# Kernel optimization log

Hardware: AMD Instinct MI355X
Metric: run time of the kernel (lower is better)

Reference implementation:

```python
import jax, jax.numpy as jnp
import numpy as np

B, T, H, V = 32, 256, 1024, 256


def setup_inputs() -> dict:
    key = jax.random.key(0)
    ks = jax.random.split(key, 12)
    xavier = float(np.sqrt(6.0 / (H + V)))
    inp = {
        "x": jax.random.randint(ks[0], (B, T), 0, V, dtype=jnp.int64),
        "targets": jax.random.randint(ks[1], (B, T), 0, V, dtype=jnp.int64),
        "h0": jnp.zeros((B, H), jnp.float32),
        "c0": jnp.zeros((B, H), jnp.float32),
        "h1": jnp.zeros((B, H), jnp.float32),
        "c1": jnp.zeros((B, H), jnp.float32),
        # learned params
        "emb": jax.random.normal(ks[2], (V, H), jnp.float32) * 0.05,
        "W_ih0": jax.random.normal(ks[3], (H, 4 * H), jnp.float32) / np.sqrt(H),
        "W_hh0": jax.random.normal(ks[4], (H, 4 * H), jnp.float32) / np.sqrt(H),
        "b0": jnp.zeros((4 * H,), jnp.float32),
        "W_ih1": jax.random.normal(ks[5], (H, 4 * H), jnp.float32) / np.sqrt(H),
        "W_hh1": jax.random.normal(ks[6], (H, 4 * H), jnp.float32) / np.sqrt(H),
        "b1": jnp.zeros((4 * H,), jnp.float32),
        "W_out": jax.random.uniform(ks[7], (H, V), jnp.float32, -xavier, xavier),
        "b_out": jnp.zeros((V,), jnp.float32),
    }
    return inp


def _lstm_cell(h, c, inp, W_ih, W_hh, b):
    # gates: [B, 4H] -> i, f, g, o
    z = inp @ W_ih + h @ W_hh + b
    i, f, g, o = jnp.split(z, 4, axis=-1)
    c_new = jax.nn.sigmoid(f) * c + jax.nn.sigmoid(i) * jnp.tanh(g)
    h_new = jax.nn.sigmoid(o) * jnp.tanh(c_new)
    return h_new, c_new


def reference(x, targets, h0, c0, h1, c1, emb, W_ih0, W_hh0, b0,
              W_ih1, W_hh1, b1, W_out, b_out):
    # Teacher-forcing branch: embed targets, feed embedding at every step.
    embeddings = emb[targets]            # [B, T, H]
    e_seq = jnp.swapaxes(embeddings, 0, 1)  # [T, B, H] for scan over time

    def step(carry, e_t):
        (h0, c0), (h1, c1) = carry
        h0, c0 = _lstm_cell(h0, c0, e_t, W_ih0, W_hh0, b0)
        h1, c1 = _lstm_cell(h1, c1, h0, W_ih1, W_hh1, b1)
        logit = h1 @ W_out + b_out       # [B, V]
        return ((h0, c0), (h1, c1)), logit

    carry0 = ((h0, c0), (h1, c1))
    carry_f, logits_tbv = jax.lax.scan(step, carry0, e_seq)
    logits = jnp.swapaxes(logits_tbv, 0, 1)  # [B, T, V]
    (h0f, c0f), (h1f, c1f) = carry_f
    return logits, h0f, c0f, h1f, c1f
```

## Files before the change

### kernel.cpp

```cpp
#include <hip/hip_runtime.h>
#include <cstdint>


typedef float    f32x4 __attribute__((ext_vector_type(4)));
typedef short    s16x8 __attribute__((ext_vector_type(8)));
typedef unsigned u32x4 __attribute__((ext_vector_type(4)));

#define DEV __device__ __forceinline__

DEV unsigned short f2bf(float x){
  unsigned u = __builtin_bit_cast(unsigned, x);
  unsigned r = (u + 0x7fffu + ((u >> 16) & 1u)) >> 16;
  return (unsigned short)r;
}
DEV float bf2f(unsigned short b){ return __builtin_bit_cast(float, ((unsigned)b) << 16); }

DEV s16x8 ld16(const void* p){ return *(const s16x8*)p; }

DEV f32x4 MF(s16x8 a, s16x8 b, f32x4 c){
  return __builtin_amdgcn_mfma_f32_16x16x32_bf16(a, b, c, 0, 0, 0);
}

#define LDC(dst, ptr)  asm volatile("global_load_dwordx4 %0, %1, off sc0 sc1" : "=v"(dst) : "v"(ptr))
#define LDP(dst, ptr)  asm volatile("global_load_dwordx4 %0, %1, off"         : "=v"(dst) : "v"(ptr))
#define WAITVM(n) do { asm volatile("s_waitcnt vmcnt(" #n ")" ::: "memory"); \
                       __builtin_amdgcn_sched_barrier(0); } while (0)
#define CFENCE()  asm volatile("" ::: "memory")
#define TRIPLE(Cmn, Ahm, Alm, Bhn, Bln) do { \
    Cmn = MF(Ahm, Bhn, Cmn); Cmn = MF(Ahm, Bln, Cmn); Cmn = MF(Alm, Bhn, Cmn); } while (0)

DEV void st16c(void* p, u32x4 v){
  asm volatile("global_store_dwordx4 %0, %1, off sc0 sc1" :: "v"(p), "v"(v) : "memory");
}
DEV void st16cf(void* p, f32x4 v){ st16c(p, __builtin_bit_cast(u32x4, v)); }
DEV void set_flag(int* p, int v){
  __hip_atomic_store(p, v, __ATOMIC_RELAXED, __HIP_MEMORY_SCOPE_AGENT);
}
template<int SLP>
DEV void pollT(const int* f, int lane, int target){
  const int* p0 = f + lane * 8;
  const int* p1 = f + (64 + lane) * 8;
  for (;;) {
    int a = __hip_atomic_load(p0, __ATOMIC_RELAXED, __HIP_MEMORY_SCOPE_AGENT);
    int b = __hip_atomic_load(p1, __ATOMIC_RELAXED, __HIP_MEMORY_SCOPE_AGENT);
    if (__all((a >= target) && (b >= target))) break;
    __builtin_amdgcn_s_sleep(SLP);
  }
  CFENCE();
}
DEV void pollC(const int* f1p, int t1, const int* f2p, int t2, int lane){
  const int* a = f1p + lane * 8;
  const int* b = f2p + lane * 8;
  for (;;) {
    int x = __hip_atomic_load(a, __ATOMIC_RELAXED, __HIP_MEMORY_SCOPE_AGENT);
    int y = __hip_atomic_load(b, __ATOMIC_RELAXED, __HIP_MEMORY_SCOPE_AGENT);
    if (__all((x >= t1) && (y >= t2))) break;
    __builtin_amdgcn_s_sleep(1);
  }
  CFENCE();
}
DEV void pollB(const int* f0p, int t0, const int* f2p, int t2,
               const int* f1p, int t1, int lane){
  const int* a0 = f0p + lane * 8;
  const int* a1 = f0p + (64 + lane) * 8;
  const int* b  = f2p + lane * 8;
  const int* c  = f1p + lane * 8;
  for (;;) {
    int x0 = __hip_atomic_load(a0, __ATOMIC_RELAXED, __HIP_MEMORY_SCOPE_AGENT);
    int x1 = __hip_atomic_load(a1, __ATOMIC_RELAXED, __HIP_MEMORY_SCOPE_AGENT);
    int y  = __hip_atomic_load(b,  __ATOMIC_RELAXED, __HIP_MEMORY_SCOPE_AGENT);
    int z  = __hip_atomic_load(c,  __ATOMIC_RELAXED, __HIP_MEMORY_SCOPE_AGENT);
    if (__all((x0 >= t0) && (x1 >= t0) && (y >= t2) && (z >= t1))) break;
    __builtin_amdgcn_s_sleep(2);
  }
  CFENCE();
}
DEV char* h0slot(char* wa0, char* s0, char* hi, int s){
  return (s == 0) ? s0 : ((s <= 128) ? wa0 + ((size_t)(s - 1) << 17)
                                     : hi  + ((size_t)(s - 129) << 17));
}

DEV void gemm16u(const char* smemA, const char* ALb, int jb0, const char* Bb,
                 int ksb, int lane, f32x4 (&C)[4][2]) {
  s16x8 P[3][4], AL[3][4];
  #pragma unroll
  for (int d = 0; d < 2; ++d) {
    #pragma unroll
    for (int q = 0; q < 4; ++q) LDP(P[d][q], Bb + ((q * 32 + ksb + d) << 10) + lane * 16);
    #pragma unroll
    for (int m = 0; m < 4; ++m)
      LDP(AL[d][m], ALb + ((((jb0 + m) * 2 + 1) * 32 + ksb + d) << 10) + lane * 16);
  }
  #pragma unroll
  for (int i = 0; i < 8; ++i) {
    const int ks = ksb + i;
    if (i < 6) {
      #pragma unroll
      for (int q = 0; q < 4; ++q) LDP(P[(i + 2) % 3][q], Bb + ((q * 32 + ks + 2) << 10) + lane * 16);
      #pragma unroll
      for (int m = 0; m < 4; ++m)
        LDP(AL[(i + 2) % 3][m], ALb + ((((jb0 + m) * 2 + 1) * 32 + ks + 2) << 10) + lane * 16);
    }
    s16x8 Ah[4];
    #pragma unroll
    for (int m = 0; m < 4; ++m) Ah[m] = ld16(smemA + ((m * 32 + ks) << 10) + lane * 16);
    if (i < 6) { WAITVM(16); } else if (i == 6) { WAITVM(8); } else { WAITVM(0); }
    #pragma unroll
    for (int m = 0; m < 4; ++m) {
      TRIPLE(C[m][0], Ah[m], AL[i % 3][m], P[i % 3][0], P[i % 3][2]);
      TRIPLE(C[m][1], Ah[m], AL[i % 3][m], P[i % 3][1], P[i % 3][3]);
    }
  }
}

__global__ void prep_wfrag(const float* __restrict__ W0, const float* __restrict__ W1,
                           const float* __restrict__ W2, const float* __restrict__ W3,
                           char* D0, char* D1, char* D2, char* D3) {
  int gid = blockIdx.x * 256 + threadIdx.x;
  int lane = gid & 63, ks = (gid >> 6) & 31, jb = (gid >> 11) & 255, mat = gid >> 19;
  const float* S = (mat == 0) ? W0 : (mat == 1) ? W1 : (mat == 2) ? W2 : W3;
  char* D = (mat == 0) ? D0 : (mat == 1) ? D1 : (mat == 2) ? D2 : D3;
  int jp = jb * 16 + (lane & 15), u = jp >> 2, g = jp & 3;
  int kb = ks * 32 + (lane >> 4) * 8;
  s16x8 vh, vl;
  #pragma unroll
  for (int i = 0; i < 8; ++i) {
    float x = S[(kb + i) * 4096 + g * 1024 + u];
    unsigned short h = f2bf(x);
    vh[i] = (short)h;
    vl[i] = (short)f2bf(x - bf2f(h));
  }
  *(s16x8*)(D + (((jb * 2 + 0) * 32 + ks) << 10) + lane * 16) = vh;
  *(s16x8*)(D + (((jb * 2 + 1) * 32 + ks) << 10) + lane * 16) = vl;
}

__global__ void prep_bfrag(const float* __restrict__ emb, const float* __restrict__ Wout,
                           char* Demb, char* Dwout) {
  int gid = blockIdx.x * 256 + threadIdx.x;
  int lane = gid & 63, ks = (gid >> 6) & 31, vb = (gid >> 11) & 15, which = gid >> 15;
  int v = vb * 16 + (lane & 15), kb = ks * 32 + (lane >> 4) * 8;
  s16x8 vh, vl;
  #pragma unroll
  for (int i = 0; i < 8; ++i) {
    float x = which ? Wout[(kb + i) * 256 + v] : emb[v * 1024 + kb + i];
    unsigned short h = f2bf(x);
    vh[i] = (short)h;
    vl[i] = (short)f2bf(x - bf2f(h));
  }
  char* D = which ? Dwout : Demb;
  *(s16x8*)(D + (((vb * 2 + 0) * 32 + ks) << 10) + lane * 16) = vh;
  *(s16x8*)(D + (((vb * 2 + 1) * 32 + ks) << 10) + lane * 16) = vl;
}

__global__ void prep_hinit(const float* __restrict__ h0, const float* __restrict__ h1,
                           char* h0s0, char* h1f) {
  int gid = blockIdx.x * 256 + threadIdx.x;
  int lane = gid & 63, ks = (gid >> 6) & 31, nt = (gid >> 11) & 1, which = gid >> 12;
  const float* S = which ? h1 : h0;
  char* D = which ? h1f : h0s0;
  int b = nt * 16 + (lane & 15), kb = ks * 32 + (lane >> 4) * 8;
  s16x8 vh, vl;
  #pragma unroll
  for (int i = 0; i < 8; ++i) {
    float x = S[b * 1024 + kb + i];
    unsigned short h = f2bf(x);
    vh[i] = (short)h;
    vl[i] = (short)f2bf(x - bf2f(h));
  }
  *(s16x8*)(D + (((0 * 2 + nt) * 32 + ks) << 10) + lane * 16) = vh;
  *(s16x8*)(D + (((1 * 2 + nt) * 32 + ks) << 10) + lane * 16) = vl;
}

__global__ void prep_misc(const float* __restrict__ b1, float* b1i,
                          int* f0a, int* f1a, int* f2a) {
  int i = blockIdx.x * 256 + threadIdx.x;
  if (i < 4096) b1i[i] = b1[(i & 3) * 1024 + (i >> 2)];
  if (i < 1024) {
    f0a[i] = -1;
    f1a[i] = (i >= 512) ? 0x7fffffff : -1;
    f2a[i] = (i >= 512) ? 0x7fffffff : -1;
  }
}

__global__ __launch_bounds__(256, 1) void lstm_persist(
    const int* __restrict__ tgt,
    const float* __restrict__ c0_in, const float* __restrict__ c1_in,
    const float* __restrict__ b0, const float* __restrict__ b_out,
    char* __restrict__ WA0, const char* __restrict__ WA1, const char* __restrict__ WA2,
    const char* __restrict__ WAi0, const char* __restrict__ WoutB, const char* __restrict__ embB,
    float* __restrict__ E0, const float* __restrict__ b1i,
    char* __restrict__ h0s0, char* __restrict__ h0hi, char* __restrict__ h1frag,
    char* __restrict__ z1ring,
    int* __restrict__ f0, int* __restrict__ f1, int* __restrict__ f2,
    float* __restrict__ out)
{
  extern __shared__ char smem[];
  constexpr int PARTA = 131072;
  constexpr int RP0   = 147456;
  constexpr int PARTB = 131072;
  constexpr int RP1   = 155648;
  const int tid = threadIdx.x, lane = tid & 63, wv = tid >> 6;
  const int wg = blockIdx.x;
  const int l15 = lane & 15, l4 = lane >> 4;

  __builtin_amdgcn_fence(__ATOMIC_ACQUIRE, "agent");

  if (wg < 128) {
    const int wgl = wg;
    const int mi_e = wv >> 1, nt_e = wv & 1;
    {
      u32x4 tmp[8];
      for (int blk = 0; blk < 4; ++blk) {
        #pragma unroll
        for (int q = 0; q < 8; ++q) {
          int idx = tid + (blk * 8 + q) * 256;
          int l16 = idx & 63, ks = (idx >> 6) & 31, mi = (idx >> 11) & 1, part = idx >> 12;
          LDC(tmp[q], WA0 + ((((wgl * 2 + mi) * 2 + part) * 32 + ks) << 10) + l16 * 16);
        }
        WAITVM(0);
        #pragma unroll
        for (int q = 0; q < 8; ++q) {
          int idx = tid + (blk * 8 + q) * 256;
          int l16 = idx & 63, ks = (idx >> 6) & 31, mi = (idx >> 11) & 1, part = idx >> 12;
          *(u32x4*)(smem + (((part * 2 + mi) * 32 + ks) << 10) + l16 * 16) = tmp[q];
        }
      }
    }
    {
      f32x4 C[2][4];
      #pragma unroll
      for (int a = 0; a < 2; ++a)
        #pragma unroll
        for (int b = 0; b < 4; ++b) C[a][b] = 0.0f;
      for (int ks = 0; ks < 32; ++ks) {
        s16x8 Ah0, Ah1, Al0, Al1;
        LDC(Ah0, WAi0 + ((((wgl * 2 + 0) * 2 + 0) * 32 + ks) << 10) + lane * 16);
        LDC(Ah1, WAi0 + ((((wgl * 2 + 1) * 2 + 0) * 32 + ks) << 10) + lane * 16);
        LDC(Al0, WAi0 + ((((wgl * 2 + 0) * 2 + 1) * 32 + ks) << 10) + lane * 16);
        LDC(Al1, WAi0 + ((((wgl * 2 + 1) * 2 + 1) * 32 + ks) << 10) + lane * 16);
        WAITVM(0);
        #pragma unroll
        for (int v4 = 0; v4 < 4; ++v4) {
          int vb = wv * 4 + v4;
          s16x8 Bh = ld16(embB + (((vb * 2 + 0) * 32 + ks) << 10) + lane * 16);
          s16x8 Bl = ld16(embB + (((vb * 2 + 1) * 32 + ks) << 10) + lane * 16);
          TRIPLE(C[0][v4], Ah0, Al0, Bh, Bl);
          TRIPLE(C[1][v4], Ah1, Al1, Bh, Bl);
        }
      }
      #pragma unroll
      for (int mi = 0; mi < 2; ++mi) {
        int jb4 = wgl * 32 + mi * 16 + l4 * 4;
        int u = jb4 >> 2;
        f32x4 bb;
        #pragma unroll
        for (int r = 0; r < 4; ++r) bb[r] = b0[r * 1024 + u];
        #pragma unroll
        for (int v4 = 0; v4 < 4; ++v4) {
          int v = (wv * 4 + v4) * 16 + l15;
          *(f32x4*)(E0 + v * 4096 + jb4) = C[mi][v4] + bb;
        }
      }
    }
    float cst = c0_in[(nt_e * 16 + l15) * 1024 + wgl * 8 + mi_e * 4 + l4];
    __syncthreads();
    if (tid == 0) set_flag(f0 + wgl * 8, 0);

    for (int t = 0; t < 256; ++t) {
      const int s = t + 1;
      f32x4 C[2][2];
      #pragma unroll
      for (int a = 0; a < 2; ++a)
        #pragma unroll
        for (int b = 0; b < 2; ++b) C[a][b] = 0.0f;
      int tv = tgt[(nt_e * 16 + l15) * 256 + t];
      f32x4 e0v = *(const f32x4*)(E0 + (size_t)tv * 4096 + wgl * 32 + mi_e * 16 + (l4 << 2));
      pollT<1>(f0, lane, t);
      const char* Bb = h0slot(WA0, h0s0, h0hi, t);
      const int ksb = wv * 8;
      s16x8 P[3][4];
      #pragma unroll
      for (int d = 0; d < 2; ++d)
        #pragma unroll
        for (int q = 0; q < 4; ++q) LDP(P[d][q], Bb + ((q * 32 + ksb + d) << 10) + lane * 16);
      #pragma unroll
      for (int i = 0; i < 8; ++i) {
        const int ks = ksb + i;
        if (i < 6) {
          #pragma unroll
          for (int q = 0; q < 4; ++q) LDP(P[(i + 2) % 3][q], Bb + ((q * 32 + ks + 2) << 10) + lane * 16);
        }
        s16x8 Ah0 = ld16(smem + ((0 * 32 + ks) << 10) + lane * 16);
        s16x8 Ah1 = ld16(smem + ((1 * 32 + ks) << 10) + lane * 16);
        s16x8 Al0 = ld16(smem + ((2 * 32 + ks) << 10) + lane * 16);
        s16x8 Al1 = ld16(smem + ((3 * 32 + ks) << 10) + lane * 16);
        if (i < 6) { WAITVM(8); } else if (i == 6) { WAITVM(4); } else { WAITVM(0); }
        TRIPLE(C[0][0], Ah0, Al0, P[i % 3][0], P[i % 3][2]);
        TRIPLE(C[0][1], Ah0, Al0, P[i % 3][1], P[i % 3][3]);
        TRIPLE(C[1][0], Ah1, Al1, P[i % 3][0], P[i % 3][2]);
        TRIPLE(C[1][1], Ah1, Al1, P[i % 3][1], P[i % 3][3]);
      }
      #pragma unroll
      for (int mi = 0; mi < 2; ++mi)
        #pragma unroll
        for (int nt = 0; nt < 2; ++nt)
          *(f32x4*)(smem + PARTA + ((wv * 4 + mi * 2 + nt) << 10) + lane * 16) = C[mi][nt];
      __syncthreads();
      {
        f32x4 z = *(const f32x4*)(smem + PARTA + ((0 * 4 + wv) << 10) + lane * 16);
        #pragma unroll
        for (int w = 1; w < 4; ++w)
          z += *(const f32x4*)(smem + PARTA + ((w * 4 + wv) << 10) + lane * 16);
        z += e0v;
        float ig = 1.f / (1.f + __expf(-z[0]));
        float fg = 1.f / (1.f + __expf(-z[1]));
        float og = 1.f / (1.f + __expf(-z[3]));
        float cn = fg * cst + ig * tanhf(z[2]);
        float hn = og * tanhf(cn);
        cst = cn;
        unsigned short hb = f2bf(hn);
        unsigned short lb = f2bf(hn - bf2f(hb));
        *(short*)(smem + RP0 + ((0 + nt_e) * 16 + l15) * 16 + (mi_e * 4 + l4) * 2) = (short)hb;
        *(short*)(smem + RP0 + ((2 + nt_e) * 16 + l15) * 16 + (mi_e * 4 + l4) * 2) = (short)lb;
        if (t == 255) {
          int u = wgl * 8 + mi_e * 4 + l4, b = nt_e * 16 + l15;
          out[2097152 + b * 1024 + u] = hn;
          out[2097152 + 32768 + b * 1024 + u] = cn;
        }
      }
      __syncthreads();
      if (wv == 0) {
        char* hd = h0slot(WA0, h0s0, h0hi, s);
        u32x4 v = *(const u32x4*)(smem + RP0 + lane * 16);
        char* dst = hd + (((lane >> 4) * 32 + (wgl >> 2)) << 10) + ((wgl & 3) * 16 + l15) * 16;
        st16c(dst, v);
        asm volatile("s_waitcnt vmcnt(0)" ::: "memory");
        if (lane == 0) set_flag(f0 + wgl * 8, s);
      }
    }
  } else if (wg < 192) {
    const int wgb = wg - 128;
    const int jb0 = wgb * 4;
    for (int idx = tid; idx < 8192; idx += 256) {
      int l16 = idx & 63, ks = (idx >> 6) & 31, m = idx >> 11;
      u32x4 v = *(const u32x4*)(WA1 + ((((jb0 + m) * 2 + 0) * 32 + ks) << 10) + l16 * 16);
      *(u32x4*)(smem + ((m * 32 + ks) << 10) + l16 * 16) = v;
    }
    __syncthreads();
    if (tid == 0) set_flag(f2 + wgb * 8, 0);

    for (int t = 0; t < 256; ++t) {
      const int rt = (t >= 4) ? (t - 3) : 0;
      pollB(f0, t + 1, f2, t, f1, rt, lane);
      f32x4 Cb[4][2];
      #pragma unroll
      for (int a = 0; a < 4; ++a)
        #pragma unroll
        for (int b = 0; b < 2; ++b) Cb[a][b] = 0.0f;
      gemm16u(smem, WA1, jb0, h0slot(WA0, h0s0, h0hi, t + 1), wv * 8, lane, Cb);
      if (wv) {
        #pragma unroll
        for (int m = 0; m < 4; ++m)
          #pragma unroll
          for (int n = 0; n < 2; ++n)
            *(f32x4*)(smem + PARTB + (((wv - 1) * 8 + m * 2 + n) << 10) + lane * 16) = Cb[m][n];
      }
      __syncthreads();
      if (wv == 0) {
        char* zs = z1ring + ((size_t)(t & 3) * 64 + wgb) * 8192;
        #pragma unroll
        for (int m = 0; m < 4; ++m)
          #pragma unroll
          for (int n = 0; n < 2; ++n) {
            f32x4 z = Cb[m][n];
            #pragma unroll
            for (int w = 1; w < 4; ++w)
              z += *(const f32x4*)(smem + PARTB + (((w - 1) * 8 + m * 2 + n) << 10) + lane * 16);
            st16cf(zs + ((m * 2 + n) * 64 + lane) * 16, z);
          }
        asm volatile("s_waitcnt vmcnt(0)" ::: "memory");
        if (lane == 0) set_flag(f2 + wgb * 8, t + 1);
      }
    }
  } else {
    const int wgc = wg - 192;
    const int jb0 = wgc * 4;
    for (int idx = tid; idx < 8192; idx += 256) {
      int l16 = idx & 63, ks = (idx >> 6) & 31, m = idx >> 11;
      u32x4 v = *(const u32x4*)(WA2 + ((((jb0 + m) * 2 + 0) * 32 + ks) << 10) + l16 * 16);
      *(u32x4*)(smem + ((m * 32 + ks) << 10) + l16 * 16) = v;
    }
    f32x4 b1z4[4];
    float cst[4][2];
    if (wv == 0) {
      #pragma unroll
      for (int m = 0; m < 4; ++m) {
        b1z4[m] = *(const f32x4*)(b1i + wgc * 64 + m * 16 + (l4 << 2));
        #pragma unroll
        for (int n = 0; n < 2; ++n)
          cst[m][n] = c1_in[(n * 16 + l15) * 1024 + wgc * 16 + m * 4 + l4];
      }
    }
    __syncthreads();
    if (tid == 0) set_flag(f1 + wgc * 8, 0);

    for (int t = 0; t < 256; ++t) {
      const int s = t + 1;
      pollC(f1, t, f2, s, lane);
      f32x4 zA[4][2];
      if (wv == 0) {
        const char* zs = z1ring + ((size_t)(t & 3) * 64 + wgc) * 8192;
        #pragma unroll
        for (int m = 0; m < 4; ++m)
          #pragma unroll
          for (int n = 0; n < 2; ++n)
            LDC(zA[m][n], zs + ((m * 2 + n) * 64 + lane) * 16);
      }
      f32x4 Cc[4][2];
      #pragma unroll
      for (int a = 0; a < 4; ++a)
        #pragma unroll
        for (int b = 0; b < 2; ++b) Cc[a][b] = 0.0f;
      gemm16u(smem, WA2, jb0, h1frag + (size_t)t * 131072, wv * 8, lane, Cc);
      if (wv) {
        #pragma unroll
        for (int m = 0; m < 4; ++m)
          #pragma unroll
          for (int n = 0; n < 2; ++n)
            *(f32x4*)(smem + PARTB + (((wv - 1) * 8 + m * 2 + n) << 10) + lane * 16) = Cc[m][n];
      }
      __syncthreads();
      if (wv == 0) {
        #pragma unroll
        for (int m = 0; m < 4; ++m)
          #pragma unroll
          for (int n = 0; n < 2; ++n) {
            f32x4 z = Cc[m][n];
            #pragma unroll
            for (int w = 1; w < 4; ++w)
              z += *(const f32x4*)(smem + PARTB + (((w - 1) * 8 + m * 2 + n) << 10) + lane * 16);
            z += zA[m][n] + b1z4[m];
            float ig = 1.f / (1.f + __expf(-z[0]));
            float fg = 1.f / (1.f + __expf(-z[1]));
            float og = 1.f / (1.f + __expf(-z[3]));
            float cn = fg * cst[m][n] + ig * tanhf(z[2]);
            float hn = og * tanhf(cn);
            cst[m][n] = cn;
            unsigned short hb = f2bf(hn);
            unsigned short lb = f2bf(hn - bf2f(hb));
            int i8 = (m * 4 + l4) & 7, subl = (m * 4 + l4) >> 3;
            *(short*)(smem + RP1 + (((0 * 2 + n) * 2 + subl) * 16 + l15) * 16 + i8 * 2) = (short)hb;
            *(short*)(smem + RP1 + (((1 * 2 + n) * 2 + subl) * 16 + l15) * 16 + i8 * 2) = (short)lb;
            if (t == 255) {
              int u = wgc * 16 + m * 4 + l4, b = n * 16 + l15;
              out[2097152 + 65536 + b * 1024 + u] = hn;
              out[2097152 + 98304 + b * 1024 + u] = cn;
            }
          }
        char* hd = h1frag + (size_t)s * 131072;
        asm volatile("s_waitcnt lgkmcnt(0)" ::: "memory");
        __builtin_amdgcn_sched_barrier(0);
        #pragma unroll
        for (int h = 0; h < 2; ++h) {
          int idx16 = lane * 2 + h;
          u32x4 v = *(const u32x4*)(smem + RP1 + idx16 * 16);
          int l15r = idx16 & 15, subl = (idx16 >> 4) & 1, ntq = (idx16 >> 5) & 1, part = idx16 >> 6;
          char* dst = hd + (((part * 2 + ntq) * 32 + (wgc >> 1)) << 10)
                         + (((wgc & 1) * 2 + subl) * 16 + l15r) * 16;
          st16c(dst, v);
        }
        asm volatile("s_waitcnt vmcnt(0)" ::: "memory");
        if (lane == 0) set_flag(f1 + wgc * 8, s);
      }
    }
  }

  {
    const int tp = wg;
    pollT<32>(f1, lane, tp + 1);
    const char* A = h1frag + (size_t)(tp + 1) * 131072;
    f32x4 C[2][4];
    #pragma unroll
    for (int a = 0; a < 2; ++a)
      #pragma unroll
      for (int b = 0; b < 4; ++b) C[a][b] = 0.0f;
    s16x8 QA[4], QB[4];
    #pragma unroll
    for (int q = 0; q < 4; ++q) LDP(QA[q], A + ((q * 32 + 0) << 10) + lane * 16);
    for (int kk = 0; kk < 16; ++kk) {
      const int ks = kk * 2;
      #pragma unroll
      for (int q = 0; q < 4; ++q) LDP(QB[q], A + ((q * 32 + ks + 1) << 10) + lane * 16);
      asm volatile("s_waitcnt vmcnt(4)" ::: "memory");
      __builtin_amdgcn_sched_barrier(0);
      #pragma unroll
      for (int v4 = 0; v4 < 4; ++v4) {
        int vb = wv * 4 + v4;
        s16x8 Bh = ld16(WoutB + (((vb * 2 + 0) * 32 + ks) << 10) + lane * 16);
        s16x8 Bl = ld16(WoutB + (((vb * 2 + 1) * 32 + ks) << 10) + lane * 16);
        C[0][v4] = MF(QA[0], Bh, C[0][v4]); C[0][v4] = MF(QA[0], Bl, C[0][v4]); C[0][v4] = MF(QA[2], Bh, C[0][v4]);
        C[1][v4] = MF(QA[1], Bh, C[1][v4]); C[1][v4] = MF(QA[1], Bl, C[1][v4]); C[1][v4] = MF(QA[3], Bh, C[1][v4]);
      }
      if (kk < 15) {
        #pragma unroll
        for (int q = 0; q < 4; ++q) LDP(QA[q], A + ((q * 32 + ks + 2) << 10) + lane * 16);
        asm volatile("s_waitcnt vmcnt(4)" ::: "memory");
      } else {
        asm volatile("s_waitcnt vmcnt(0)" ::: "memory");
      }
      __builtin_amdgcn_sched_barrier(0);
      #pragma unroll
      for (int v4 = 0; v4 < 4; ++v4) {
        int vb = wv * 4 + v4;
        s16x8 Bh = ld16(WoutB + (((vb * 2 + 0) * 32 + ks + 1) << 10) + lane * 16);
        s16x8 Bl = ld16(WoutB + (((vb * 2 + 1) * 32 + ks + 1) << 10) + lane * 16);
        C[0][v4] = MF(QB[0], Bh, C[0][v4]); C[0][v4] = MF(QB[0], Bl, C[0][v4]); C[0][v4] = MF(QB[2], Bh, C[0][v4]);
        C[1][v4] = MF(QB[1], Bh, C[1][v4]); C[1][v4] = MF(QB[1], Bl, C[1][v4]); C[1][v4] = MF(QB[3], Bh, C[1][v4]);
      }
    }
    #pragma unroll
    for (int nt = 0; nt < 2; ++nt)
      #pragma unroll
      for (int v4 = 0; v4 < 4; ++v4) {
        int v = (wv * 4 + v4) * 16 + l15;
        float bo = b_out[v];
        #pragma unroll
        for (int r = 0; r < 4; ++r) {
          int b = nt * 16 + l4 * 4 + r;
          out[((size_t)b * 256 + tp) * 256 + v] = C[nt][v4][r] + bo;
        }
      }
  }
}

extern "C" void kernel_launch(void* const* d_in, const int* in_sizes, int n_in,
                              void* d_out, int out_size, void* d_ws, size_t ws_size,
                              hipStream_t stream) {
  const int*   targets = (const int*)d_in[1];
  const float* h0_in   = (const float*)d_in[2];
  const float* c0_in   = (const float*)d_in[3];
  const float* h1_in   = (const float*)d_in[4];
  const float* c1_in   = (const float*)d_in[5];
  const float* emb     = (const float*)d_in[6];
  const float* W_ih0   = (const float*)d_in[7];
  const float* W_hh0   = (const float*)d_in[8];
  const float* b0      = (const float*)d_in[9];
  const float* W_ih1   = (const float*)d_in[10];
  const float* W_hh1   = (const float*)d_in[11];
  const float* b1      = (const float*)d_in[12];
  const float* W_out   = (const float*)d_in[13];
  const float* b_out   = (const float*)d_in[14];
  float* out = (float*)d_out;

  char* ws = (char*)d_ws;
  char*  WA0    = ws;
  char*  WA1    = ws + 16777216;
  char*  WA2    = ws + 33554432;
  char*  WoutB  = ws + 50331648;
  char*  embB   = ws + 51380224;
  float* E0     = (float*)(ws + 52428800);
  float* b1i    = (float*)(ws + 56623104);
  int*   f0     = (int*)(ws + 56639488);
  int*   f1     = (int*)(ws + 56643584);
  char*  h0s0   = ws + 56647680;
  char*  h0hi   = ws + 56778752;
  char*  h1frag = ws + 73555968;
  char*  z1ring = ws + 107241472;
  int*   f2     = (int*)(ws + 109338624);
  char*  WAi0   = h1frag + 16777216;

  prep_misc <<<18,   256, 0, stream>>>(b1, b1i, f0, f1, f2);
  prep_wfrag<<<8192, 256, 0, stream>>>(W_hh0, W_ih1, W_hh1, W_ih0, WA0, WA1, WA2, WAi0);
  prep_bfrag<<<256,  256, 0, stream>>>(emb, W_out, embB, WoutB);
  prep_hinit<<<32,   256, 0, stream>>>(h0_in, h1_in, h0s0, h1frag);

  hipFuncSetAttribute(reinterpret_cast<const void*>(lstm_persist),
                      hipFuncAttributeMaxDynamicSharedMemorySize, 157696);
  lstm_persist<<<256, 256, 157696, stream>>>(
      targets, c0_in, c1_in, b0, b_out,
      WA0, WA1, WA2, WAi0, WoutB, embB,
      E0, b1i, h0s0, h0hi, h1frag, z1ring, f0, f1, f2, out);
}
```

Baseline: 2.106 ms.

## Rebalance persistent LSTM roles: fewer layer-0 blocks, more layer-1 recurrent blocks

Reassigns the 256 persistent workgroups so that layer 0 uses 64 blocks, each owning 64 gate columns, while the layer-1 recurrent stage uses 128 blocks with 32 columns each. Before this, layer 0 had 128 blocks and layer-1 recurrence had 64. Layer-0 blocks now run the shared gemm16u routine over a 4-tile slice of W_hh0. Layer-1 blocks use the split-K pipelined inner loop with hi/lo weights held in LDS. Workspace slots, flag layouts and poll helpers are rearranged to match, including h1 history slots placed in reused weight buffers. The aim is to shorten the layer-1 recurrent critical path, at the cost of more work per layer-0 block, which could lengthen layer 0's recurrence instead.

```diff
diff --git a/kernel.cpp b/kernel.cpp
--- a/kernel.cpp
+++ b/kernel.cpp
@@ -35,6 +35,16 @@
 DEV void st16cf(void* p, f32x4 v){ st16c(p, __builtin_bit_cast(u32x4, v)); }
 DEV void set_flag(int* p, int v){
   __hip_atomic_store(p, v, __ATOMIC_RELAXED, __HIP_MEMORY_SCOPE_AGENT);
+}
+template<int SLP>
+DEV void poll64(const int* f, int lane, int target){
+  const int* p = f + lane * 8;
+  for (;;) {
+    int a = __hip_atomic_load(p, __ATOMIC_RELAXED, __HIP_MEMORY_SCOPE_AGENT);
+    if (__all(a >= target)) break;
+    __builtin_amdgcn_s_sleep(SLP);
+  }
+  CFENCE();
 }
 template<int SLP>
 DEV void pollT(const int* f, int lane, int target){
@@ -48,36 +58,34 @@
   }
   CFENCE();
 }
-DEV void pollC(const int* f1p, int t1, const int* f2p, int t2, int lane){
-  const int* a = f1p + lane * 8;
-  const int* b = f2p + lane * 8;
-  for (;;) {
-    int x = __hip_atomic_load(a, __ATOMIC_RELAXED, __HIP_MEMORY_SCOPE_AGENT);
-    int y = __hip_atomic_load(b, __ATOMIC_RELAXED, __HIP_MEMORY_SCOPE_AGENT);
-    if (__all((x >= t1) && (y >= t2))) break;
-    __builtin_amdgcn_s_sleep(1);
-  }
-  CFENCE();
-}
 DEV void pollB(const int* f0p, int t0, const int* f2p, int t2,
                const int* f1p, int t1, int lane){
-  const int* a0 = f0p + lane * 8;
-  const int* a1 = f0p + (64 + lane) * 8;
+  const int* a = f0p + lane * 8;
+  const int* b = f2p + lane * 8;
+  const int* c0 = f1p + lane * 8;
+  const int* c1 = f1p + (64 + lane) * 8;
+  for (;;) {
+    int x = __hip_atomic_load(a,  __ATOMIC_RELAXED, __HIP_MEMORY_SCOPE_AGENT);
+    int y = __hip_atomic_load(b,  __ATOMIC_RELAXED, __HIP_MEMORY_SCOPE_AGENT);
+    int z0 = __hip_atomic_load(c0, __ATOMIC_RELAXED, __HIP_MEMORY_SCOPE_AGENT);
+    int z1 = __hip_atomic_load(c1, __ATOMIC_RELAXED, __HIP_MEMORY_SCOPE_AGENT);
+    if (__all((x >= t0) && (y >= t2) && (z0 >= t1) && (z1 >= t1))) break;
+    __builtin_amdgcn_s_sleep(2);
+  }
+  CFENCE();
+}
+DEV void pollC(const int* f1p, int t1, const int* f2p, int t2, int lane){
+  const int* a0 = f1p + lane * 8;
+  const int* a1 = f1p + (64 + lane) * 8;
   const int* b  = f2p + lane * 8;
-  const int* c  = f1p + lane * 8;
   for (;;) {
     int x0 = __hip_atomic_load(a0, __ATOMIC_RELAXED, __HIP_MEMORY_SCOPE_AGENT);
     int x1 = __hip_atomic_load(a1, __ATOMIC_RELAXED, __HIP_MEMORY_SCOPE_AGENT);
     int y  = __hip_atomic_load(b,  __ATOMIC_RELAXED, __HIP_MEMORY_SCOPE_AGENT);
-    int z  = __hip_atomic_load(c,  __ATOMIC_RELAXED, __HIP_MEMORY_SCOPE_AGENT);
-    if (__all((x0 >= t0) && (x1 >= t0) && (y >= t2) && (z >= t1))) break;
-    __builtin_amdgcn_s_sleep(2);
+    if (__all((x0 >= t1) && (x1 >= t1) && (y >= t2))) break;
+    __builtin_amdgcn_s_sleep(1);
   }
   CFENCE();
-}
-DEV char* h0slot(char* wa0, char* s0, char* hi, int s){
-  return (s == 0) ? s0 : ((s <= 128) ? wa0 + ((size_t)(s - 1) << 17)
-                                     : hi  + ((size_t)(s - 129) << 17));
 }
 
 DEV void gemm16u(const char* smemA, const char* ALb, int jb0, const char* Bb,
@@ -153,11 +161,11 @@
 }
 
 __global__ void prep_hinit(const float* __restrict__ h0, const float* __restrict__ h1,
-                           char* h0s0, char* h1f) {
+                           char* h0s0, char* h1s0) {
   int gid = blockIdx.x * 256 + threadIdx.x;
   int lane = gid & 63, ks = (gid >> 6) & 31, nt = (gid >> 11) & 1, which = gid >> 12;
   const float* S = which ? h1 : h0;
-  char* D = which ? h1f : h0s0;
+  char* D = which ? h1s0 : h0s0;
   int b = nt * 16 + (lane & 15), kb = ks * 32 + (lane >> 4) * 8;
   s16x8 vh, vl;
   #pragma unroll
@@ -175,82 +183,70 @@
                           int* f0a, int* f1a, int* f2a) {
   int i = blockIdx.x * 256 + threadIdx.x;
   if (i < 4096) b1i[i] = b1[(i & 3) * 1024 + (i >> 2)];
-  if (i < 1024) {
-    f0a[i] = -1;
-    f1a[i] = (i >= 512) ? 0x7fffffff : -1;
-    f2a[i] = (i >= 512) ? 0x7fffffff : -1;
-  }
+  if (i < 1024) { f0a[i] = -1; f1a[i] = -1; f2a[i] = -1; }
 }
 
 __global__ __launch_bounds__(256, 1) void lstm_persist(
     const int* __restrict__ tgt,
     const float* __restrict__ c0_in, const float* __restrict__ c1_in,
     const float* __restrict__ b0, const float* __restrict__ b_out,
-    char* __restrict__ WA0, const char* __restrict__ WA1, const char* __restrict__ WA2,
-    const char* __restrict__ WAi0, const char* __restrict__ WoutB, const char* __restrict__ embB,
+    const char* __restrict__ WA0, const char* __restrict__ WA1, char* __restrict__ WA2,
+    char* __restrict__ WAi0, const char* __restrict__ WoutB, const char* __restrict__ embB,
     float* __restrict__ E0, const float* __restrict__ b1i,
-    char* __restrict__ h0s0, char* __restrict__ h0hi, char* __restrict__ h1frag,
-    char* __restrict__ z1ring,
+    char* __restrict__ h0all, char* __restrict__ h1s0, char* __restrict__ z1ring,
     int* __restrict__ f0, int* __restrict__ f1, int* __restrict__ f2,
     float* __restrict__ out)
 {
   extern __shared__ char smem[];
-  constexpr int PARTA = 131072;
-  constexpr int RP0   = 147456;
-  constexpr int PARTB = 131072;
-  constexpr int RP1   = 155648;
+  constexpr int PARTAB = 131072;
+  constexpr int RPA    = 155648;
+  constexpr int PARTC  = 131072;
+  constexpr int RPC    = 143360;
   const int tid = threadIdx.x, lane = tid & 63, wv = tid >> 6;
   const int wg = blockIdx.x;
   const int l15 = lane & 15, l4 = lane >> 4;
 
+  auto h1slot = [&](int s) -> char* {
+    return (s == 0) ? h1s0 : ((s <= 128) ? WA2 + ((size_t)(s - 1) << 17)
+                                         : WAi0 + ((size_t)(s - 129) << 17));
+  };
+  auto h0slot = [&](int s) -> char* { return h0all + ((size_t)s << 17); };
+
   __builtin_amdgcn_fence(__ATOMIC_ACQUIRE, "agent");
 
-  if (wg < 128) {
+  if (wg < 64) {
     const int wgl = wg;
-    const int mi_e = wv >> 1, nt_e = wv & 1;
+    for (int idx = tid; idx < 8192; idx += 256) {
+      int l16 = idx & 63, ks = (idx >> 6) & 31, m = idx >> 11;
+      u32x4 v = *(const u32x4*)(WA0 + ((((wgl * 4 + m) * 2 + 0) * 32 + ks) << 10) + l16 * 16);
+      *(u32x4*)(smem + ((m * 32 + ks) << 10) + l16 * 16) = v;
+    }
     {
-      u32x4 tmp[8];
-      for (int blk = 0; blk < 4; ++blk) {
-        #pragma unroll
-        for (int q = 0; q < 8; ++q) {
-          int idx = tid + (blk * 8 + q) * 256;
-          int l16 = idx & 63, ks = (idx >> 6) & 31, mi = (idx >> 11) & 1, part = idx >> 12;
-          LDC(tmp[q], WA0 + ((((wgl * 2 + mi) * 2 + part) * 32 + ks) << 10) + l16 * 16);
-        }
-        WAITVM(0);
-        #pragma unroll
-        for (int q = 0; q < 8; ++q) {
-          int idx = tid + (blk * 8 + q) * 256;
-          int l16 = idx & 63, ks = (idx >> 6) & 31, mi = (idx >> 11) & 1, part = idx >> 12;
-          *(u32x4*)(smem + (((part * 2 + mi) * 32 + ks) << 10) + l16 * 16) = tmp[q];
-        }
-      }
-    }
-    {
-      f32x4 C[2][4];
-      #pragma unroll
-      for (int a = 0; a < 2; ++a)
+      f32x4 C[4][4];
+      #pragma unroll
+      for (int a = 0; a < 4; ++a)
         #pragma unroll
         for (int b = 0; b < 4; ++b) C[a][b] = 0.0f;
       for (int ks = 0; ks < 32; ++ks) {
-        s16x8 Ah0, Ah1, Al0, Al1;
-        LDC(Ah0, WAi0 + ((((wgl * 2 + 0) * 2 + 0) * 32 + ks) << 10) + lane * 16);
-        LDC(Ah1, WAi0 + ((((wgl * 2 + 1) * 2 + 0) * 32 + ks) << 10) + lane * 16);
-        LDC(Al0, WAi0 + ((((wgl * 2 + 0) * 2 + 1) * 32 + ks) << 10) + lane * 16);
-        LDC(Al1, WAi0 + ((((wgl * 2 + 1) * 2 + 1) * 32 + ks) << 10) + lane * 16);
+        s16x8 Ah[4], Al[4];
+        #pragma unroll
+        for (int m = 0; m < 4; ++m) {
+          LDC(Ah[m], WAi0 + ((((wgl * 4 + m) * 2 + 0) * 32 + ks) << 10) + lane * 16);
+          LDC(Al[m], WAi0 + ((((wgl * 4 + m) * 2 + 1) * 32 + ks) << 10) + lane * 16);
+        }
         WAITVM(0);
         #pragma unroll
         for (int v4 = 0; v4 < 4; ++v4) {
           int vb = wv * 4 + v4;
           s16x8 Bh = ld16(embB + (((vb * 2 + 0) * 32 + ks) << 10) + lane * 16);
           s16x8 Bl = ld16(embB + (((vb * 2 + 1) * 32 + ks) << 10) + lane * 16);
-          TRIPLE(C[0][v4], Ah0, Al0, Bh, Bl);
-          TRIPLE(C[1][v4], Ah1, Al1, Bh, Bl);
-        }
-      }
-      #pragma unroll
-      for (int mi = 0; mi < 2; ++mi) {
-        int jb4 = wgl * 32 + mi * 16 + l4 * 4;
+          #pragma unroll
+          for (int m = 0; m < 4; ++m) TRIPLE(C[m][v4], Ah[m], Al[m], Bh, Bl);
+        }
+      }
+      #pragma unroll
+      for (int m = 0; m < 4; ++m) {
+        int jb4 = wgl * 64 + m * 16 + l4 * 4;
         int u = jb4 >> 2;
         f32x4 bb;
         #pragma unroll
@@ -258,188 +254,58 @@
         #pragma unroll
         for (int v4 = 0; v4 < 4; ++v4) {
           int v = (wv * 4 + v4) * 16 + l15;
-          *(f32x4*)(E0 + v * 4096 + jb4) = C[mi][v4] + bb;
-        }
-      }
-    }
-    float cst = c0_in[(nt_e * 16 + l15) * 1024 + wgl * 8 + mi_e * 4 + l4];
+          *(f32x4*)(E0 + v * 4096 + jb4) = C[m][v4] + bb;
+        }
+      }
+    }
+    float cst[4][2];
+    if (wv == 0) {
+      #pragma unroll
+      for (int m = 0; m < 4; ++m)
+        #pragma unroll
+        for (int n = 0; n < 2; ++n)
+          cst[m][n] = c0_in[(n * 16 + l15) * 1024 + wgl * 16 + m * 4 + l4];
+    }
     __syncthreads();
     if (tid == 0) set_flag(f0 + wgl * 8, 0);
 
     for (int t = 0; t < 256; ++t) {
       const int s = t + 1;
-      f32x4 C[2][2];
-      #pragma unroll
-      for (int a = 0; a < 2; ++a)
+      f32x4 e0v[4][2];
+      if (wv == 0) {
+        #pragma unroll
+        for (int n = 0; n < 2; ++n) {
+          int tv = tgt[(n * 16 + l15) * 256 + t];
+          #pragma unroll
+          for (int m = 0; m < 4; ++m)
+            e0v[m][n] = *(const f32x4*)(E0 + (size_t)tv * 4096 + wgl * 64 + m * 16 + (l4 << 2));
+        }
+      }
+      poll64<1>(f0, lane, t);
+      f32x4 C[4][2];
+      #pragma unroll
+      for (int a = 0; a < 4; ++a)
         #pragma unroll
         for (int b = 0; b < 2; ++b) C[a][b] = 0.0f;
-      int tv = tgt[(nt_e * 16 + l15) * 256 + t];
-      f32x4 e0v = *(const f32x4*)(E0 + (size_t)tv * 4096 + wgl * 32 + mi_e * 16 + (l4 << 2));
-      pollT<1>(f0, lane, t);
-      const char* Bb = h0slot(WA0, h0s0, h0hi, t);
-      const int ksb = wv * 8;
-      s16x8 P[3][4];
-      #pragma unroll
-      for (int d = 0; d < 2; ++d)
-        #pragma unroll
-        for (int q = 0; q < 4; ++q) LDP(P[d][q], Bb + ((q * 32 + ksb + d) << 10) + lane * 16);
-      #pragma unroll
-      for (int i = 0; i < 8; ++i) {
-        const int ks = ksb + i;
-        if (i < 6) {
-          #pragma unroll
-          for (int q = 0; q < 4; ++q) LDP(P[(i + 2) % 3][q], Bb + ((q * 32 + ks + 2) << 10) + lane * 16);
-        }
-        s16x8 Ah0 = ld16(smem + ((0 * 32 + ks) << 10) + lane * 16);
-        s16x8 Ah1 = ld16(smem + ((1 * 32 + ks) << 10) + lane * 16);
-        s16x8 Al0 = ld16(smem + ((2 * 32 + ks) << 10) + lane * 16);
-        s16x8 Al1 = ld16(smem + ((3 * 32 + ks) << 10) + lane * 16);
-        if (i < 6) { WAITVM(8); } else if (i == 6) { WAITVM(4); } else { WAITVM(0); }
-        TRIPLE(C[0][0], Ah0, Al0, P[i % 3][0], P[i % 3][2]);
-        TRIPLE(C[0][1], Ah0, Al0, P[i % 3][1], P[i % 3][3]);
-        TRIPLE(C[1][0], Ah1, Al1, P[i % 3][0], P[i % 3][2]);
-        TRIPLE(C[1][1], Ah1, Al1, P[i % 3][1], P[i % 3][3]);
-      }
-      #pragma unroll
-      for (int mi = 0; mi < 2; ++mi)
-        #pragma unroll
-        for (int nt = 0; nt < 2; ++nt)
-          *(f32x4*)(smem + PARTA + ((wv * 4 + mi * 2 + nt) << 10) + lane * 16) = C[mi][nt];
-      __syncthreads();
-      {
-        f32x4 z = *(const f32x4*)(smem + PARTA + ((0 * 4 + wv) << 10) + lane * 16);
-        #pragma unroll
-        for (int w = 1; w < 4; ++w)
-          z += *(const f32x4*)(smem + PARTA + ((w * 4 + wv) << 10) + lane * 16);
-        z += e0v;
-        float ig = 1.f / (1.f + __expf(-z[0]));
-        float fg = 1.f / (1.f + __expf(-z[1]));
-        float og = 1.f / (1.f + __expf(-z[3]));
-        float cn = fg * cst + ig * tanhf(z[2]);
-        float hn = og * tanhf(cn);
-        cst = cn;
-        unsigned short hb = f2bf(hn);
-        unsigned short lb = f2bf(hn - bf2f(hb));
-        *(short*)(smem + RP0 + ((0 + nt_e) * 16 + l15) * 16 + (mi_e * 4 + l4) * 2) = (short)hb;
-        *(short*)(smem + RP0 + ((2 + nt_e) * 16 + l15) * 16 + (mi_e * 4 + l4) * 2) = (short)lb;
-        if (t == 255) {
-          int u = wgl * 8 + mi_e * 4 + l4, b = nt_e * 16 + l15;
-          out[2097152 + b * 1024 + u] = hn;
-          out[2097152 + 32768 + b * 1024 + u] = cn;
-        }
+      gemm16u(smem, WA0, wgl * 4, h0slot(t), wv * 8, lane, C);
+      if (wv) {
+        #pragma unroll
+        for (int m = 0; m < 4; ++m)
+          #pragma unroll
+          for (int n = 0; n < 2; ++n)
+            *(f32x4*)(smem + PARTAB + (((wv - 1) * 8 + m * 2 + n) << 10) + lane * 16) = C[m][n];
       }
       __syncthreads();
       if (wv == 0) {
-        char* hd = h0slot(WA0, h0s0, h0hi, s);
-        u32x4 v = *(const u32x4*)(smem + RP0 + lane * 16);
-        char* dst = hd + (((lane >> 4) * 32 + (wgl >> 2)) << 10) + ((wgl & 3) * 16 + l15) * 16;
-        st16c(dst, v);
-        asm volatile("s_waitcnt vmcnt(0)" ::: "memory");
-        if (lane == 0) set_flag(f0 + wgl * 8, s);
-      }
-    }
-  } else if (wg < 192) {
-    const int wgb = wg - 128;
-    const int jb0 = wgb * 4;
-    for (int idx = tid; idx < 8192; idx += 256) {
-      int l16 = idx & 63, ks = (idx >> 6) & 31, m = idx >> 11;
-      u32x4 v = *(const u32x4*)(WA1 + ((((jb0 + m) * 2 + 0) * 32 + ks) << 10) + l16 * 16);
-      *(u32x4*)(smem + ((m * 32 + ks) << 10) + l16 * 16) = v;
-    }
-    __syncthreads();
-    if (tid == 0) set_flag(f2 + wgb * 8, 0);
-
-    for (int t = 0; t < 256; ++t) {
-      const int rt = (t >= 4) ? (t - 3) : 0;
-      pollB(f0, t + 1, f2, t, f1, rt, lane);
-      f32x4 Cb[4][2];
-      #pragma unroll
-      for (int a = 0; a < 4; ++a)
-        #pragma unroll
-        for (int b = 0; b < 2; ++b) Cb[a][b] = 0.0f;
-      gemm16u(smem, WA1, jb0, h0slot(WA0, h0s0, h0hi, t + 1), wv * 8, lane, Cb);
-      if (wv) {
         #pragma unroll
         for (int m = 0; m < 4; ++m)
           #pragma unroll
-          for (int n = 0; n < 2; ++n)
-            *(f32x4*)(smem + PARTB + (((wv - 1) * 8 + m * 2 + n) << 10) + lane * 16) = Cb[m][n];
-      }
-      __syncthreads();
-      if (wv == 0) {
-        char* zs = z1ring + ((size_t)(t & 3) * 64 + wgb) * 8192;
-        #pragma unroll
-        for (int m = 0; m < 4; ++m)
-          #pragma unroll
           for (int n = 0; n < 2; ++n) {
-            f32x4 z = Cb[m][n];
+            f32x4 z = C[m][n];
             #pragma unroll
             for (int w = 1; w < 4; ++w)
-              z += *(const f32x4*)(smem + PARTB + (((w - 1) * 8 + m * 2 + n) << 10) + lane * 16);
-            st16cf(zs + ((m * 2 + n) * 64 + lane) * 16, z);
-          }
-        asm volatile("s_waitcnt vmcnt(0)" ::: "memory");
-        if (lane == 0) set_flag(f2 + wgb * 8, t + 1);
-      }
-    }
-  } else {
-    const int wgc = wg - 192;
-    const int jb0 = wgc * 4;
-    for (int idx = tid; idx < 8192; idx += 256) {
-      int l16 = idx & 63, ks = (idx >> 6) & 31, m = idx >> 11;
-      u32x4 v = *(const u32x4*)(WA2 + ((((jb0 + m) * 2 + 0) * 32 + ks) << 10) + l16 * 16);
-      *(u32x4*)(smem + ((m * 32 + ks) << 10) + l16 * 16) = v;
-    }
-    f32x4 b1z4[4];
-    float cst[4][2];
-    if (wv == 0) {
-      #pragma unroll
-      for (int m = 0; m < 4; ++m) {
-        b1z4[m] = *(const f32x4*)(b1i + wgc * 64 + m * 16 + (l4 << 2));
-        #pragma unroll
-        for (int n = 0; n < 2; ++n)
-          cst[m][n] = c1_in[(n * 16 + l15) * 1024 + wgc * 16 + m * 4 + l4];
-      }
-    }
-    __syncthreads();
-    if (tid == 0) set_flag(f1 + wgc * 8, 0);
-
-    for (int t = 0; t < 256; ++t) {
-      const int s = t + 1;
-      pollC(f1, t, f2, s, lane);
-      f32x4 zA[4][2];
-      if (wv == 0) {
-        const char* zs = z1ring + ((size_t)(t & 3) * 64 + wgc) * 8192;
-        #pragma unroll
-        for (int m = 0; m < 4; ++m)
-          #pragma unroll
-          for (int n = 0; n < 2; ++n)
-            LDC(zA[m][n], zs + ((m * 2 + n) * 64 + lane) * 16);
-      }
-      f32x4 Cc[4][2];
-      #pragma unroll
-      for (int a = 0; a < 4; ++a)
-        #pragma unroll
-        for (int b = 0; b < 2; ++b) Cc[a][b] = 0.0f;
-      gemm16u(smem, WA2, jb0, h1frag + (size_t)t * 131072, wv * 8, lane, Cc);
-      if (wv) {
-        #pragma unroll
-        for (int m = 0; m < 4; ++m)
-          #pragma unroll
-          for (int n = 0; n < 2; ++n)
-            *(f32x4*)(smem + PARTB + (((wv - 1) * 8 + m * 2 + n) << 10) + lane * 16) = Cc[m][n];
-      }
-      __syncthreads();
-      if (wv == 0) {
-        #pragma unroll
-        for (int m = 0; m < 4; ++m)
-          #pragma unroll
-          for (int n = 0; n < 2; ++n) {
-            f32x4 z = Cc[m][n];
-            #pragma unroll
-            for (int w = 1; w < 4; ++w)
-              z += *(const f32x4*)(smem + PARTB + (((w - 1) * 8 + m * 2 + n) << 10) + lane * 16);
-            z += zA[m][n] + b1z4[m];
+              z += *(const f32x4*)(smem + PARTAB + (((w - 1) * 8 + m * 2 + n) << 10) + lane * 16);
+            z += e0v[m][n];
             float ig = 1.f / (1.f + __expf(-z[0]));
             float fg = 1.f / (1.f + __expf(-z[1]));
             float og = 1.f / (1.f + __expf(-z[3]));
@@ -448,27 +314,193 @@
             cst[m][n] = cn;
             unsigned short hb = f2bf(hn);
             unsigned short lb = f2bf(hn - bf2f(hb));
-            int i8 = (m * 4 + l4) & 7, subl = (m * 4 + l4) >> 3;
-            *(short*)(smem + RP1 + (((0 * 2 + n) * 2 + subl) * 16 + l15) * 16 + i8 * 2) = (short)hb;
-            *(short*)(smem + RP1 + (((1 * 2 + n) * 2 + subl) * 16 + l15) * 16 + i8 * 2) = (short)lb;
+            int ul = m * 4 + l4, j8 = ul >> 3, i8 = ul & 7;
+            *(short*)(smem + RPA + (((0 * 2 + n) * 2 + j8) * 16 + l15) * 16 + i8 * 2) = (short)hb;
+            *(short*)(smem + RPA + (((1 * 2 + n) * 2 + j8) * 16 + l15) * 16 + i8 * 2) = (short)lb;
             if (t == 255) {
-              int u = wgc * 16 + m * 4 + l4, b = n * 16 + l15;
+              int u = wgl * 16 + ul, b = n * 16 + l15;
+              out[2097152 + b * 1024 + u] = hn;
+              out[2097152 + 32768 + b * 1024 + u] = cn;
+            }
+          }
+        char* hd = h0slot(s);
+        asm volatile("s_waitcnt lgkmcnt(0)" ::: "memory");
+        __builtin_amdgcn_sched_barrier(0);
+        #pragma unroll
+        for (int h = 0; h < 2; ++h) {
+          int idx16 = lane * 2 + h;
+          u32x4 v = *(const u32x4*)(smem + RPA + idx16 * 16);
+          int l15r = idx16 & 15, subl = (idx16 >> 4) & 1, ntq = (idx16 >> 5) & 1, part = idx16 >> 6;
+          char* dst = hd + (((part * 2 + ntq) * 32 + (wgl >> 1)) << 10)
+                         + (((wgl & 1) * 2 + subl) * 16 + l15r) * 16;
+          st16c(dst, v);
+        }
+        asm volatile("s_waitcnt vmcnt(0)" ::: "memory");
+        if (lane == 0) set_flag(f0 + wgl * 8, s);
+      }
+    }
+  } else if (wg < 128) {
+    const int wgb = wg - 64;
+    const int jb0 = wgb * 4;
+    for (int idx = tid; idx < 8192; idx += 256) {
+      int l16 = idx & 63, ks = (idx >> 6) & 31, m = idx >> 11;
+      u32x4 v = *(const u32x4*)(WA1 + ((((jb0 + m) * 2 + 0) * 32 + ks) << 10) + l16 * 16);
+      *(u32x4*)(smem + ((m * 32 + ks) << 10) + l16 * 16) = v;
+    }
+    __syncthreads();
+    if (tid == 0) set_flag(f2 + wgb * 8, 0);
+
+    for (int t = 0; t < 256; ++t) {
+      pollB(f0, t + 1, f2, t, f1, t - 3, lane);
+      f32x4 Cb[4][2];
+      #pragma unroll
+      for (int a = 0; a < 4; ++a)
+        #pragma unroll
+        for (int b = 0; b < 2; ++b) Cb[a][b] = 0.0f;
+      gemm16u(smem, WA1, jb0, h0slot(t + 1), wv * 8, lane, Cb);
+      if (wv) {
+        #pragma unroll
+        for (int m = 0; m < 4; ++m)
+          #pragma unroll
+          for (int n = 0; n < 2; ++n)
+            *(f32x4*)(smem + PARTAB + (((wv - 1) * 8 + m * 2 + n) << 10) + lane * 16) = Cb[m][n];
+      }
+      __syncthreads();
+      if (wv == 0) {
+        char* zs = z1ring + ((size_t)(t & 3) * 64 + wgb) * 8192;
+        #pragma unroll
+        for (int m = 0; m < 4; ++m)
+          #pragma unroll
+          for (int n = 0; n < 2; ++n) {
+            f32x4 z = Cb[m][n];
+            #pragma unroll
+            for (int w = 1; w < 4; ++w)
+              z += *(const f32x4*)(smem + PARTAB + (((w - 1) * 8 + m * 2 + n) << 10) + lane * 16);
+            st16cf(zs + ((m * 2 + n) * 64 + lane) * 16, z);
+          }
+        asm volatile("s_waitcnt vmcnt(0)" ::: "memory");
+        if (lane == 0) set_flag(f2 + wgb * 8, t + 1);
+      }
+    }
+  } else {
+    const int wgc = wg - 128;
+    {
+      u32x4 tmp[8];
+      for (int blk = 0; blk < 4; ++blk) {
+        #pragma unroll
+        for (int q = 0; q < 8; ++q) {
+          int idx = tid + (blk * 8 + q) * 256;
+          int l16 = idx & 63, ks = (idx >> 6) & 31, mi = (idx >> 11) & 1, part = idx >> 12;
+          LDC(tmp[q], WA2 + ((((wgc * 2 + mi) * 2 + part) * 32 + ks) << 10) + l16 * 16);
+        }
+        WAITVM(0);
+        #pragma unroll
+        for (int q = 0; q < 8; ++q) {
+          int idx = tid + (blk * 8 + q) * 256;
+          int l16 = idx & 63, ks = (idx >> 6) & 31, mi = (idx >> 11) & 1, part = idx >> 12;
+          *(u32x4*)(smem + (((part * 2 + mi) * 32 + ks) << 10) + l16 * 16) = tmp[q];
+        }
+      }
+    }
+    f32x4 b1z[2];
+    float cst[2][2];
+    if (wv == 0) {
+      #pragma unroll
+      for (int mi = 0; mi < 2; ++mi) {
+        b1z[mi] = *(const f32x4*)(b1i + wgc * 32 + mi * 16 + (l4 << 2));
+        #pragma unroll
+        for (int nt = 0; nt < 2; ++nt)
+          cst[mi][nt] = c1_in[(nt * 16 + l15) * 1024 + wgc * 8 + mi * 4 + l4];
+      }
+    }
+    __syncthreads();
+    if (tid == 0) set_flag(f1 + wgc * 8, 0);
+
+    for (int t = 0; t < 256; ++t) {
+      const int s = t + 1;
+      pollC(f1, t, f2, s, lane);
+      f32x4 zA[2][2];
+      if (wv == 0) {
+        const char* zs = z1ring + ((size_t)(t & 3) * 64 + (wgc >> 1)) * 8192;
+        #pragma unroll
+        for (int mi = 0; mi < 2; ++mi) {
+          int mb = (wgc & 1) * 2 + mi;
+          #pragma unroll
+          for (int nt = 0; nt < 2; ++nt)
+            LDC(zA[mi][nt], zs + ((mb * 2 + nt) * 64 + lane) * 16);
+        }
+      }
+      f32x4 C[2][2];
+      #pragma unroll
+      for (int a = 0; a < 2; ++a)
+        #pragma unroll
+        for (int b = 0; b < 2; ++b) C[a][b] = 0.0f;
+      {
+        const char* Bb = h1slot(t);
+        const int ksb = wv * 8;
+        s16x8 P[3][4];
+        #pragma unroll
+        for (int d = 0; d < 2; ++d)
+          #pragma unroll
+          for (int q = 0; q < 4; ++q) LDP(P[d][q], Bb + ((q * 32 + ksb + d) << 10) + lane * 16);
+        #pragma unroll
+        for (int i = 0; i < 8; ++i) {
+          const int ks = ksb + i;
+          if (i < 6) {
+            #pragma unroll
+            for (int q = 0; q < 4; ++q) LDP(P[(i + 2) % 3][q], Bb + ((q * 32 + ks + 2) << 10) + lane * 16);
+          }
+          s16x8 Ah0 = ld16(smem + ((0 * 32 + ks) << 10) + lane * 16);
+          s16x8 Ah1 = ld16(smem + ((1 * 32 + ks) << 10) + lane * 16);
+          s16x8 Al0 = ld16(smem + ((2 * 32 + ks) << 10) + lane * 16);
+          s16x8 Al1 = ld16(smem + ((3 * 32 + ks) << 10) + lane * 16);
+          if (i < 6) { WAITVM(8); } else if (i == 6) { WAITVM(4); } else { WAITVM(0); }
+          TRIPLE(C[0][0], Ah0, Al0, P[i % 3][0], P[i % 3][2]);
+          TRIPLE(C[0][1], Ah0, Al0, P[i % 3][1], P[i % 3][3]);
+          TRIPLE(C[1][0], Ah1, Al1, P[i % 3][0], P[i % 3][2]);
+          TRIPLE(C[1][1], Ah1, Al1, P[i % 3][1], P[i % 3][3]);
+        }
+      }
+      if (wv) {
+        #pragma unroll
+        for (int mi = 0; mi < 2; ++mi)
+          #pragma unroll
+          for (int nt = 0; nt < 2; ++nt)
+            *(f32x4*)(smem + PARTC + (((wv - 1) * 4 + mi * 2 + nt) << 10) + lane * 16) = C[mi][nt];
+      }
+      __syncthreads();
+      if (wv == 0) {
+        #pragma unroll
+        for (int mi = 0; mi < 2; ++mi)
+          #pragma unroll
+          for (int nt = 0; nt < 2; ++nt) {
+            f32x4 z = C[mi][nt];
+            #pragma unroll
+            for (int w = 1; w < 4; ++w)
+              z += *(const f32x4*)(smem + PARTC + (((w - 1) * 4 + mi * 2 + nt) << 10) + lane * 16);
+            z += zA[mi][nt] + b1z[mi];
+            float ig = 1.f / (1.f + __expf(-z[0]));
+            float fg = 1.f / (1.f + __expf(-z[1]));
+            float og = 1.f / (1.f + __expf(-z[3]));
+            float cn = fg * cst[mi][nt] + ig * tanhf(z[2]);
+            float hn = og * tanhf(cn);
+            cst[mi][nt] = cn;
+            unsigned short hb = f2bf(hn);
+            unsigned short lb = f2bf(hn - bf2f(hb));
+            *(short*)(smem + RPC + ((0 + nt) * 16 + l15) * 16 + (mi * 4 + l4) * 2) = (short)hb;
+            *(short*)(smem + RPC + ((2 + nt) * 16 + l15) * 16 + (mi * 4 + l4) * 2) = (short)lb;
+            if (t == 255) {
+              int u = wgc * 8 + mi * 4 + l4, b = nt * 16 + l15;
               out[2097152 + 65536 + b * 1024 + u] = hn;
               out[2097152 + 98304 + b * 1024 + u] = cn;
             }
           }
-        char* hd = h1frag + (size_t)s * 131072;
+        char* hd = h1slot(s);
         asm volatile("s_waitcnt lgkmcnt(0)" ::: "memory");
         __builtin_amdgcn_sched_barrier(0);
-        #pragma unroll
-        for (int h = 0; h < 2; ++h) {
-          int idx16 = lane * 2 + h;
-          u32x4 v = *(const u32x4*)(smem + RP1 + idx16 * 16);
-          int l15r = idx16 & 15, subl = (idx16 >> 4) & 1, ntq = (idx16 >> 5) & 1, part = idx16 >> 6;
-          char* dst = hd + (((part * 2 + ntq) * 32 + (wgc >> 1)) << 10)
-                         + (((wgc & 1) * 2 + subl) * 16 + l15r) * 16;
-          st16c(dst, v);
-        }
+        u32x4 v = *(const u32x4*)(smem + RPC + lane * 16);
+        char* dst = hd + (((lane >> 4) * 32 + (wgc >> 2)) << 10) + ((wgc & 3) * 16 + l15) * 16;
+        st16c(dst, v);
         asm volatile("s_waitcnt vmcnt(0)" ::: "memory");
         if (lane == 0) set_flag(f1 + wgc * 8, s);
       }
@@ -478,7 +510,7 @@
   {
     const int tp = wg;
     pollT<32>(f1, lane, tp + 1);
-    const char* A = h1frag + (size_t)(tp + 1) * 131072;
+    const char* A = h1slot(tp + 1);
     f32x4 C[2][4];
     #pragma unroll
     for (int a = 0; a < 2; ++a)
@@ -556,28 +588,27 @@
   char*  WA0    = ws;
   char*  WA1    = ws + 16777216;
   char*  WA2    = ws + 33554432;
-  char*  WoutB  = ws + 50331648;
-  char*  embB   = ws + 51380224;
-  float* E0     = (float*)(ws + 52428800);
-  float* b1i    = (float*)(ws + 56623104);
-  int*   f0     = (int*)(ws + 56639488);
-  int*   f1     = (int*)(ws + 56643584);
-  char*  h0s0   = ws + 56647680;
-  char*  h0hi   = ws + 56778752;
-  char*  h1frag = ws + 73555968;
-  char*  z1ring = ws + 107241472;
-  int*   f2     = (int*)(ws + 109338624);
-  char*  WAi0   = h1frag + 16777216;
+  char*  WAi0   = ws + 50331648;
+  char*  WoutB  = ws + 67108864;
+  char*  embB   = ws + 68157440;
+  float* E0     = (float*)(ws + 69206016);
+  float* b1i    = (float*)(ws + 73400320);
+  int*   f0     = (int*)(ws + 73416704);
+  int*   f1     = (int*)(ws + 73420800);
+  int*   f2     = (int*)(ws + 73424896);
+  char*  h0all  = ws + 73428992;
+  char*  h1s0   = ws + 107114496;
+  char*  z1ring = ws + 107245568;
 
   prep_misc <<<18,   256, 0, stream>>>(b1, b1i, f0, f1, f2);
   prep_wfrag<<<8192, 256, 0, stream>>>(W_hh0, W_ih1, W_hh1, W_ih0, WA0, WA1, WA2, WAi0);
   prep_bfrag<<<256,  256, 0, stream>>>(emb, W_out, embB, WoutB);
-  prep_hinit<<<32,   256, 0, stream>>>(h0_in, h1_in, h0s0, h1frag);
+  prep_hinit<<<32,   256, 0, stream>>>(h0_in, h1_in, h0all, h1s0);
 
   hipFuncSetAttribute(reinterpret_cast<const void*>(lstm_persist),
                       hipFuncAttributeMaxDynamicSharedMemorySize, 157696);
   lstm_persist<<<256, 256, 157696, stream>>>(
       targets, c0_in, c1_in, b0, b_out,
       WA0, WA1, WA2, WAi0, WoutB, embB,
-      E0, b1i, h0s0, h0hi, h1frag, z1ring, f0, f1, f2, out);
-}
+      E0, b1i, h0all, h1s0, z1ring, f0, f1, f2, out);
+}
```

Result: faster. 2.008 ms (-4.7%).
